# Kernel optimization log

Hardware: AMD Instinct MI355X
Metric: run time of the kernel (lower is better)

Reference implementation:

```python
import jax, jax.numpy as jnp
import numpy as np

N = 10000       # nodes (= number of eigenpairs)
NFEAT = 512
NCLASS = 64     # hidden size of attention/FFN when norm='none'
HID = 128       # feat_encoder hidden
DIM = 32        # eig encoder hidden_dim
K = 10          # outer loop count of ParamNonHarmonicEncoding
NF = DIM // 2   # num_freq = 16
OMEGA = 50.0
DMIN = 0.25
NLAYER = 1


def _ln(x, g, b, eps=1e-5):
    m = jnp.mean(x, axis=-1, keepdims=True)
    v = jnp.mean((x - m) ** 2, axis=-1, keepdims=True)
    return g * (x - m) / jnp.sqrt(v + eps) + b


def setup_inputs() -> dict:
    key = jax.random.key(0)
    ks = jax.random.split(key, 32)
    f32 = jnp.float32
    def w(k, shape, s=0.05):
        return jax.random.normal(k, shape, dtype=f32) * s
    inp = {
        "e": jax.random.uniform(ks[0], (N,), dtype=f32),
        "u": jax.random.normal(ks[1], (N, N), dtype=f32) / np.float32(np.sqrt(N)),
        "x": jax.random.normal(ks[2], (N, NFEAT), dtype=f32),
        # feat_encoder: Linear(nfeat,hid) -> ReLU -> Linear(hid,nclass)
        "fe_w1": w(ks[3], (NFEAT, HID)), "fe_b1": jnp.zeros((HID,), f32),
        "fe_w2": w(ks[4], (HID, NCLASS)), "fe_b2": jnp.zeros((NCLASS,), f32),
        # ParamNonHarmonicEncoding
        "freq_deltas": jax.random.uniform(ks[5], (NF,), dtype=f32) * 0.5,
        "freq_bias": jnp.zeros((), f32),
        "readout_w": w(ks[6], (K, 1 + 2 * NF), 0.1),
        "readout_b": jnp.zeros((K,), f32),
        "alpha_w": w(ks[7], (K, 1), 0.3),   # nn.Linear(k,1,bias=False)
        # mha pre-norm
        "mha_ln_g": jnp.ones((NCLASS,), f32), "mha_ln_b": jnp.zeros((NCLASS,), f32),
        # Diff attention (H=1, hidden=nclass)
        "wq1": w(ks[8], (NCLASS, NCLASS)), "bq1": jnp.zeros((NCLASS,), f32),
        "wk1": w(ks[9], (NCLASS, NCLASS)), "bk1": jnp.zeros((NCLASS,), f32),
        "wq2": w(ks[10], (NCLASS, NCLASS)), "bq2": jnp.zeros((NCLASS,), f32),
        "wk2": w(ks[11], (NCLASS, NCLASS)), "bk2": jnp.zeros((NCLASS,), f32),
        "wv": w(ks[12], (NCLASS, NCLASS)), "bv": jnp.zeros((NCLASS,), f32),
        "lq1": w(ks[13], (NCLASS,), 0.1), "lk1": w(ks[14], (NCLASS,), 0.1),
        "lq2": w(ks[15], (NCLASS,), 0.1), "lk2": w(ks[16], (NCLASS,), 0.1),
        "attn_ln_g": jnp.ones((NCLASS,), f32), "attn_ln_b": jnp.zeros((NCLASS,), f32),
        "out_w": w(ks[17], (NCLASS, NCLASS)), "out_b": jnp.zeros((NCLASS,), f32),
        # gating
        "gate_ln_g": jnp.ones((3 * NCLASS,), f32), "gate_ln_b": jnp.zeros((3 * NCLASS,), f32),
        "gate_w": w(ks[18], (3 * NCLASS, 3)), "gate_b": jnp.zeros((3,), f32),
        # FFN
        "ffn_ln_g": jnp.ones((NCLASS,), f32), "ffn_ln_b": jnp.zeros((NCLASS,), f32),
        "ffn_w1": w(ks[19], (NCLASS, NCLASS)), "ffn_b1": jnp.zeros((NCLASS,), f32),
        "ffn_w2": w(ks[20], (NCLASS, NCLASS)), "ffn_b2": jnp.zeros((NCLASS,), f32),
    }
    return inp


def reference(e, u, x, fe_w1, fe_b1, fe_w2, fe_b2,
              freq_deltas, freq_bias, readout_w, readout_b, alpha_w,
              mha_ln_g, mha_ln_b,
              wq1, bq1, wk1, bk1, wq2, bq2, wk2, bk2, wv, bv,
              lq1, lk1, lq2, lk2, attn_ln_g, attn_ln_b, out_w, out_b,
              gate_ln_g, gate_ln_b, gate_w, gate_b,
              ffn_ln_g, ffn_ln_b, ffn_w1, ffn_b1, ffn_w2, ffn_b2):
    # feat encoder (all dropouts are 0 / eval mode)
    h = jnp.maximum(x @ fe_w1 + fe_b1, 0.0) @ fe_w2 + fe_b2          # [N, C]

    # ParamNonHarmonicEncoding, vectorized over the k powers
    deltas = jax.nn.softplus(freq_deltas) + DMIN
    freqs = jnp.cumsum(deltas) + freq_bias
    freqs = OMEGA * jnp.tanh(freqs / OMEGA)                           # [F]
    powers = e[:, None] ** jnp.arange(1, K + 1, dtype=e.dtype)        # [N, K]
    phase = powers[:, :, None] * freqs                                # [N, K, F]
    ns = jnp.asarray(NF ** 0.5, e.dtype)
    feat = jnp.concatenate(
        [jnp.ones_like(powers)[..., None], jnp.sin(phase) / ns, jnp.cos(phase) / ns],
        axis=-1)                                                      # [N, K, 1+2F]
    eig = jnp.einsum('nkf,kf->nk', feat, readout_w) + readout_b      # [N, K]
    new_e = eig @ alpha_w                                             # [N, 1]

    for layer in range(NLAYER):
        # spectral propagation: u @ diag-like(new_e) @ u^T @ h
        utx = u.T @ h                                                 # [N, C]
        h_fur = u @ (new_e * utx)                                     # [N, C]

        # differential linear attention
        mh = _ln(h, mha_ln_g, mha_ln_b)
        q1 = mh @ wq1 + bq1; k1 = mh @ wk1 + bk1
        q2 = mh @ wq2 + bq2; k2 = mh @ wk2 + bk2
        v = mh @ wv + bv
        k1v = k1.T @ v                                                # [C, C]
        k2v = k2.T @ v
        lam1 = jnp.exp(jnp.sum(lq1 * lk1))
        lam2 = jnp.exp(jnp.sum(lq2 * lk2))
        lam_init = 0.8 - 0.6 * float(np.exp(-0.3 * layer))
        lam_full = lam1 - lam2 + lam_init
        xa = q1 @ k1v - (q2 @ k2v) * lam_full
        xa = _ln(xa, attn_ln_g, attn_ln_b) * (1.0 - lam_init)
        mha_h = xa @ out_w + out_b                                    # [N, C]

        # gated mixing
        cat = jnp.concatenate([h, mha_h, h_fur], axis=-1)             # [N, 3C]
        g = jax.nn.softmax(_ln(cat, gate_ln_g, gate_ln_b) @ gate_w + gate_b, axis=-1)
        mix = h * g[:, 0:1] + mha_h * g[:, 1:2] + h_fur * g[:, 2:3]

        f = _ln(mix, ffn_ln_g, ffn_ln_b)
        f = jax.nn.gelu(f @ ffn_w1 + ffn_b1, approximate=False) @ ffn_w2 + ffn_b2
        h = mix + f
    return h
```

## Files before the change

kernel.cpp:

```cpp
#include <hip/hip_runtime.h>
#include <hip/hip_bf16.h>
#include <math.h>

#define NN 10000
#define J48 10048
#define CHUNKS 157
#define CPS 20
#define SPLITS 8

typedef __bf16 bf16;
typedef bf16 bf16x8 __attribute__((ext_vector_type(8)));
typedef float f32x4 __attribute__((ext_vector_type(4)));

#define SYNC_LDS() do {                                      \
    asm volatile("s_waitcnt lgkmcnt(0)" ::: "memory");       \
    __builtin_amdgcn_sched_barrier(0);                       \
    __builtin_amdgcn_s_barrier();                            \
    __builtin_amdgcn_sched_barrier(0);                       \
  } while (0)

__device__ __forceinline__ float wave_sum64(float v) {
#pragma unroll
  for (int m = 32; m >= 1; m >>= 1) v += __shfl_xor(v, m, 64);
  return v;
}

__global__ void prep_kernel(const float* __restrict__ w1, const float* __restrict__ w2,
                            const float* __restrict__ wq1, const float* __restrict__ wk1,
                            const float* __restrict__ wq2, const float* __restrict__ wk2,
                            const float* __restrict__ wvw,
                            const float* __restrict__ bq1, const float* __restrict__ bk1,
                            const float* __restrict__ bq2, const float* __restrict__ bk2,
                            const float* __restrict__ bvv,
                            const float* __restrict__ lq1, const float* __restrict__ lk1,
                            const float* __restrict__ lq2, const float* __restrict__ lk2,
                            const float* __restrict__ freq_deltas, const float* __restrict__ freq_bias,
                            bf16* __restrict__ w1T, bf16* __restrict__ w2T, bf16* __restrict__ qkvT,
                            float* __restrict__ bqkv, float* __restrict__ freqs, float* __restrict__ lamb) {
  int tid = blockIdx.x * blockDim.x + threadIdx.x;
  int nthr = gridDim.x * blockDim.x;
  for (int i = tid; i < 512 * 128; i += nthr) {
    int o = i >> 9, k = i & 511;
    w1T[i] = (bf16)w1[k * 128 + o];
  }
  for (int i = tid; i < 64 * 128; i += nthr) {
    int o = i >> 7, k = i & 127;
    w2T[i] = (bf16)w2[k * 64 + o];
  }
  for (int i = tid; i < 320 * 64; i += nthr) {
    int r = i >> 6, k = i & 63;
    const float* W = (r < 64) ? wq1 : (r < 128) ? wk1 : (r < 192) ? wq2 : (r < 256) ? wk2 : wvw;
    qkvT[i] = (bf16)W[k * 64 + (r & 63)];
  }
  for (int i = tid; i < 320; i += nthr) {
    const float* B = (i < 64) ? bq1 : (i < 128) ? bk1 : (i < 192) ? bq2 : (i < 256) ? bk2 : bvv;
    bqkv[i] = B[i & 63];
  }
  if (blockIdx.x == 0) {
    if (threadIdx.x == 0) {
      float acc = freq_bias[0];
      for (int f = 0; f < 16; f++) {
        acc += log1pf(expf(freq_deltas[f])) + 0.25f;
        freqs[f] = 50.0f * tanhf(acc * (1.0f / 50.0f));
      }
    }
    if (threadIdx.x >= 64 && threadIdx.x < 128) {
      int l = threadIdx.x - 64;
      float s1 = wave_sum64(lq1[l] * lk1[l]);
      float s2 = wave_sum64(lq2[l] * lk2[l]);
      if (l == 0) lamb[0] = expf(s1) - expf(s2) + 0.2f;
    }
  }
}

__global__ void newe_kernel(const float* __restrict__ e, const float* __restrict__ rw,
                            const float* __restrict__ rb, const float* __restrict__ aw,
                            const float* __restrict__ freqs, float* __restrict__ newe) {
  int n = blockIdx.x * blockDim.x + threadIdx.x;
  if (n >= NN) return;
  float fr[16];
#pragma unroll
  for (int f = 0; f < 16; f++) fr[f] = freqs[f];
  float ev = e[n], p = 1.0f, acc = 0.0f;
  for (int k = 0; k < 10; k++) {
    p *= ev;
    float s = rb[k] + rw[k * 33];
#pragma unroll
    for (int f = 0; f < 16; f++) {
      float ph = p * fr[f];
      s += 0.25f * (__sinf(ph) * rw[k * 33 + 1 + f] + __cosf(ph) * rw[k * 33 + 17 + f]);
    }
    acc += s * aw[k];
  }
  newe[n] = acc;
}

__global__ __launch_bounds__(256) void g1_kernel(const float* __restrict__ x, const bf16* __restrict__ w1T,
                                                 const float* __restrict__ b1, bf16* __restrict__ t1b) {
  __shared__ bf16 la[64][40];
  __shared__ bf16 lb[128][40];
  const int bm = blockIdx.x * 64;
  const int lane = threadIdx.x & 63, wvid = threadIdx.x >> 6;
  const int am = threadIdx.x >> 2, aseg = (threadIdx.x & 3) * 8;
  const int arow = bm + am;
  f32x4 acc[8] = {};
  float4 aLo, aHi;
  uint4 bChunk[2];
  auto fetchAll = [&](int k0) {
    if (arow < NN) {
      const float4* p = (const float4*)(x + (size_t)arow * 512 + k0 + aseg);
      aLo = p[0]; aHi = p[1];
    } else {
      aLo = make_float4(0.f, 0.f, 0.f, 0.f); aHi = aLo;
    }
#pragma unroll
    for (int r = 0; r < 2; r++) {
      int slot = threadIdx.x * 2 + r;
      int n = slot >> 2, seg = (slot & 3) * 8;
      bChunk[r] = *(const uint4*)(w1T + n * 512 + k0 + seg);
    }
  };
  auto store = [&]() {
    union { uint4 v; bf16 b[8]; } pk;
    float av[8] = {aLo.x, aLo.y, aLo.z, aLo.w, aHi.x, aHi.y, aHi.z, aHi.w};
#pragma unroll
    for (int t = 0; t < 8; t++) pk.b[t] = (bf16)av[t];
    *(uint4*)&la[am][aseg] = pk.v;
#pragma unroll
    for (int r = 0; r < 2; r++) {
      int slot = threadIdx.x * 2 + r;
      int n = slot >> 2, seg = (slot & 3) * 8;
      *(uint4*)&lb[n][seg] = bChunk[r];
    }
  };
  fetchAll(0);
  for (int k0 = 0; k0 < 512; k0 += 32) {
    store();
    if (k0 + 32 < 512) fetchAll(k0 + 32);
    __syncthreads();
    bf16x8 af = *(const bf16x8*)&la[wvid * 16 + (lane & 15)][(lane >> 4) * 8];
#pragma unroll
    for (int s = 0; s < 8; s++) {
      bf16x8 bfr = *(const bf16x8*)&lb[s * 16 + (lane & 15)][(lane >> 4) * 8];
      acc[s] = __builtin_amdgcn_mfma_f32_16x16x32_bf16(af, bfr, acc[s], 0, 0, 0);
    }
    __syncthreads();
  }
#pragma unroll
  for (int s = 0; s < 8; s++) {
    int col = s * 16 + (lane & 15);
    float bvv = b1[col];
#pragma unroll
    for (int r = 0; r < 4; r++) {
      int row = bm + wvid * 16 + (lane >> 4) * 4 + r;
      if (row < NN) {
        float v = acc[s][r] + bvv;
        t1b[(size_t)row * 128 + col] = (bf16)(v > 0.f ? v : 0.f);
      }
    }
  }
}

__global__ __launch_bounds__(256) void g2_kernel(const bf16* __restrict__ t1b, const bf16* __restrict__ w2T,
                                                 const float* __restrict__ b2, const float* __restrict__ lng,
                                                 const float* __restrict__ lnb, float* __restrict__ h,
                                                 bf16* __restrict__ hT, bf16* __restrict__ mh) {
  __shared__ bf16 la[64][72];
  __shared__ bf16 lb[64][72];
  const int bm = blockIdx.x * 64;
  const int lane = threadIdx.x & 63, wvid = threadIdx.x >> 6;
  f32x4 acc[4] = {};
  for (int k0 = 0; k0 < 128; k0 += 64) {
#pragma unroll
    for (int r = 0; r < 2; r++) {
      int slot = threadIdx.x * 2 + r;
      int m = slot >> 3, seg = (slot & 7) * 8;
      int row = bm + m;
      uint4 val = make_uint4(0u, 0u, 0u, 0u);
      if (row < NN) val = *(const uint4*)(t1b + (size_t)row * 128 + k0 + seg);
      *(uint4*)&la[m][seg] = val;
      *(uint4*)&lb[m][seg] = *(const uint4*)(w2T + m * 128 + k0 + seg);
    }
    __syncthreads();
#pragma unroll
    for (int ks = 0; ks < 2; ks++) {
      bf16x8 af = *(const bf16x8*)&la[wvid * 16 + (lane & 15)][ks * 32 + (lane >> 4) * 8];
#pragma unroll
      for (int s = 0; s < 4; s++) {
        bf16x8 bfr = *(const bf16x8*)&lb[s * 16 + (lane & 15)][ks * 32 + (lane >> 4) * 8];
        acc[s] = __builtin_amdgcn_mfma_f32_16x16x32_bf16(af, bfr, acc[s], 0, 0, 0);
      }
    }
    __syncthreads();
  }
  float bv4[4], g4[4], lb4[4];
#pragma unroll
  for (int s = 0; s < 4; s++) {
    int col = s * 16 + (lane & 15);
    bv4[s] = b2[col]; g4[s] = lng[col]; lb4[s] = lnb[col];
  }
#pragma unroll
  for (int r = 0; r < 4; r++) {
    float vals[4], psum = 0.f;
#pragma unroll
    for (int s = 0; s < 4; s++) { vals[s] = acc[s][r] + bv4[s]; psum += vals[s]; }
#pragma unroll
    for (int msk = 1; msk < 16; msk <<= 1) psum += __shfl_xor(psum, msk, 64);
    float mean = psum * (1.0f / 64.0f);
    float pvar = 0.f;
#pragma unroll
    for (int s = 0; s < 4; s++) { float dd = vals[s] - mean; pvar += dd * dd; }
#pragma unroll
    for (int msk = 1; msk < 16; msk <<= 1) pvar += __shfl_xor(pvar, msk, 64);
    float rsq = rsqrtf(pvar * (1.0f / 64.0f) + 1e-5f);
    int row = bm + wvid * 16 + (lane >> 4) * 4 + r;
    if (row < NN) {
#pragma unroll
      for (int s = 0; s < 4; s++) {
        int col = s * 16 + (lane & 15);
        float v = vals[s];
        h[(size_t)row * 64 + col] = v;
        hT[(size_t)col * NN + row] = (bf16)v;
        mh[(size_t)row * 64 + col] = (bf16)(g4[s] * (v - mean) * rsq + lb4[s]);
      }
    }
  }
}

__global__ __launch_bounds__(256) void qkv_kernel(const bf16* __restrict__ mh, const bf16* __restrict__ qkvT,
                                                  const float* __restrict__ bqkv,
                                                  bf16* __restrict__ qq, bf16* __restrict__ kv) {
  __shared__ bf16 la[64][72];
  __shared__ bf16 lb[320][72];
  const int bm = blockIdx.x * 64;
  const int lane = threadIdx.x & 63, wvid = threadIdx.x >> 6;
#pragma unroll
  for (int r = 0; r < 2; r++) {
    int slot = threadIdx.x * 2 + r;
    int m = slot >> 3, seg = (slot & 7) * 8;
    int row = bm + m;
    uint4 val = make_uint4(0u, 0u, 0u, 0u);
    if (row < NN) val = *(const uint4*)(mh + (size_t)row * 64 + seg);
    *(uint4*)&la[m][seg] = val;
  }
#pragma unroll
  for (int r = 0; r < 10; r++) {
    int slot = threadIdx.x * 10 + r;
    int n = slot >> 3, seg = (slot & 7) * 8;
    *(uint4*)&lb[n][seg] = *(const uint4*)(qkvT + n * 64 + seg);
  }
  __syncthreads();
  f32x4 acc[20] = {};
#pragma unroll
  for (int ks = 0; ks < 2; ks++) {
    bf16x8 af = *(const bf16x8*)&la[wvid * 16 + (lane & 15)][ks * 32 + (lane >> 4) * 8];
#pragma unroll
    for (int s = 0; s < 20; s++) {
      bf16x8 bfr = *(const bf16x8*)&lb[s * 16 + (lane & 15)][ks * 32 + (lane >> 4) * 8];
      acc[s] = __builtin_amdgcn_mfma_f32_16x16x32_bf16(af, bfr, acc[s], 0, 0, 0);
    }
  }
#pragma unroll
  for (int s = 0; s < 20; s++) {
    int col = s * 16 + (lane & 15);
    float bvv = bqkv[col];
    bf16* dst; int dc, stride;
    if (col < 64)       { dst = qq; dc = col;       stride = 128; }
    else if (col < 128) { dst = kv; dc = col - 64;  stride = 192; }
    else if (col < 192) { dst = qq; dc = col - 64;  stride = 128; }
    else                { dst = kv; dc = col - 128; stride = 192; }
#pragma unroll
    for (int r = 0; r < 4; r++) {
      int row = bm + wvid * 16 + (lane >> 4) * 4 + r;
      if (row < NN) dst[(size_t)row * stride + dc] = (bf16)(acc[s][r] + bvv);
    }
  }
}

__global__ __launch_bounds__(256) void r1_kernel(const bf16* __restrict__ kv, float* __restrict__ part) {
  int b = blockIdx.x;
  int c1 = threadIdx.x & 63, grp = threadIdx.x >> 6;
  int r0 = b * 16;
  float a1[16] = {}, a2[16] = {};
  for (int r = 0; r < 16; r++) {
    const bf16* rowp = kv + (size_t)(r0 + r) * 192;
    float k1 = (float)rowp[c1];
    float k2 = (float)rowp[64 + c1];
    union { uint4 v; bf16 b[8]; } v0, v1;
    v0.v = *(const uint4*)(rowp + 128 + grp * 16);
    v1.v = *(const uint4*)(rowp + 136 + grp * 16);
#pragma unroll
    for (int q = 0; q < 8; q++) {
      float va = (float)v0.b[q], vb = (float)v1.b[q];
      a1[q] += k1 * va; a2[q] += k2 * va;
      a1[8 + q] += k1 * vb; a2[8 + q] += k2 * vb;
    }
  }
  float* p1 = part + (size_t)b * 8192 + (size_t)c1 * 64 + grp * 16;
  float* p2 = p1 + 4096;
#pragma unroll
  for (int q = 0; q < 16; q++) { p1[q] = a1[q]; p2[q] = a2[q]; }
}

__global__ __launch_bounds__(256) void r2a_kernel(const float* __restrict__ part, float* __restrict__ part2) {
  int flat = blockIdx.x * 256 + threadIdx.x;
  int y = blockIdx.y;
  int b0 = y * 79, b1 = min(625, b0 + 79);
  float s = 0.f;
  for (int b = b0; b < b1; b++) s += part[(size_t)b * 8192 + flat];
  part2[(size_t)flat * 8 + y] = s;
}

__global__ void r2b_kernel(const float* __restrict__ part2, const float* __restrict__ lamb, bf16* __restrict__ Bt) {
  int flat = blockIdx.x * 256 + threadIdx.x;
  int mat = flat >> 12, rem = flat & 4095;
  int d = rem >> 6, c = rem & 63;
  f32x4 lo = *(const f32x4*)(part2 + (size_t)flat * 8);
  f32x4 hi = *(const f32x4*)(part2 + (size_t)flat * 8 + 4);
  float s = lo[0] + lo[1] + lo[2] + lo[3] + hi[0] + hi[1] + hi[2] + hi[3];
  float v = mat ? (-lamb[0] * s) : s;
  Bt[c * 128 + mat * 64 + d] = (bf16)v;
}

__global__ __launch_bounds__(256) void d_split_kernel(const float* __restrict__ u, const bf16* __restrict__ hT,
                                                      float* __restrict__ dpart) {
  __shared__ bf16 la[64][72];
  __shared__ bf16 lb[64][72];
  const int j0 = blockIdx.x * 64;
  const int sk = blockIdx.y;
  const int c0 = sk * CPS, c1e = min(CHUNKS, c0 + CPS);
  const int t = threadIdx.x;
  const int lane = t & 63, wv = t >> 6;
  const int jl = (t & 15) * 4;
  const int ir = (t >> 4) * 4;
  f32x4 acc[4] = {};
  uint4 aC[2];
  float4 bC[4];
  auto fetchAll = [&](int i0) {
#pragma unroll
    for (int r = 0; r < 2; r++) {
      int slot = t * 2 + r;
      int c = slot >> 3, seg = (slot & 7) * 8;
      int i = i0 + seg;
      if (i + 7 < NN) aC[r] = *(const uint4*)(hT + (size_t)c * NN + i);
      else {
        union { uint4 v; bf16 b[8]; } tu;
#pragma unroll
        for (int q = 0; q < 8; q++) tu.b[q] = (i + q < NN) ? hT[(size_t)c * NN + i + q] : (bf16)0.f;
        aC[r] = tu.v;
      }
    }
#pragma unroll
    for (int q = 0; q < 4; q++) {
      int i = i0 + ir + q;
      if (i < NN && (j0 + jl + 3) < NN) bC[q] = *(const float4*)(u + (size_t)i * NN + j0 + jl);
      else if (i < NN) {
        float tmp[4];
#pragma unroll
        for (int q2 = 0; q2 < 4; q2++) tmp[q2] = (j0 + jl + q2 < NN) ? u[(size_t)i * NN + j0 + jl + q2] : 0.f;
        bC[q] = make_float4(tmp[0], tmp[1], tmp[2], tmp[3]);
      } else bC[q] = make_float4(0.f, 0.f, 0.f, 0.f);
    }
  };
  auto storeAll = [&]() {
#pragma unroll
    for (int r = 0; r < 2; r++) {
      int slot = t * 2 + r;
      int c = slot >> 3, seg = (slot & 7) * 8;
      *(uint4*)&la[c][seg] = aC[r];
    }
#pragma unroll
    for (int q2 = 0; q2 < 4; q2++) {
      int j = jl + q2;
      int isw = ir ^ (((j >> 2) & 3) << 3);
      union { uint2 w; bf16 b[4]; } pk;
      pk.b[0] = (bf16)((float*)&bC[0])[q2];
      pk.b[1] = (bf16)((float*)&bC[1])[q2];
      pk.b[2] = (bf16)((float*)&bC[2])[q2];
      pk.b[3] = (bf16)((float*)&bC[3])[q2];
      *(uint2*)&lb[j][isw] = pk.w;
    }
  };
  fetchAll(c0 * 64);
  for (int ch = c0; ch < c1e; ch++) {
    storeAll();
    if (ch + 1 < c1e) fetchAll((ch + 1) * 64);
    SYNC_LDS();
#pragma unroll
    for (int ks = 0; ks < 2; ks++) {
      bf16x8 af = *(const bf16x8*)&la[wv * 16 + (lane & 15)][ks * 32 + (lane >> 4) * 8];
#pragma unroll
      for (int s = 0; s < 4; s++) {
        int j = s * 16 + (lane & 15);
        int ioff = (ks * 32 + (lane >> 4) * 8) ^ (((j >> 2) & 3) << 3);
        bf16x8 bfr = *(const bf16x8*)&lb[j][ioff];
        acc[s] = __builtin_amdgcn_mfma_f32_16x16x32_bf16(af, bfr, acc[s], 0, 0, 0);
      }
    }
    SYNC_LDS();
  }
#pragma unroll
  for (int s = 0; s < 4; s++) {
    int j = j0 + s * 16 + (lane & 15);
#pragma unroll
    for (int r = 0; r < 4; r++) {
      int c = wv * 16 + (lane >> 4) * 4 + r;
      dpart[((size_t)sk * 64 + c) * J48 + j] = acc[s][r];
    }
  }
}

__global__ void dred_kernel(const float* __restrict__ dpart, const float* __restrict__ newe,
                            bf16* __restrict__ wutxT) {
  int idx = blockIdx.x * 256 + threadIdx.x;
  int c = idx / 2512;
  int j = (idx - c * 2512) * 4;
  if (c >= 64 || j >= NN) return;
  f32x4 s = {};
  for (int sk = 0; sk < SPLITS; sk++)
    s += *(const f32x4*)(dpart + ((size_t)sk * 64 + c) * J48 + j);
  union { uint2 w; bf16 b[4]; } pk;
#pragma unroll
  for (int q = 0; q < 4; q++) pk.b[q] = (bf16)(newe[j + q] * s[q]);
  *(uint2*)&wutxT[(size_t)c * NN + j] = pk.w;
}

__global__ __launch_bounds__(256) void e_split_kernel(const float* __restrict__ u, const bf16* __restrict__ wutxT,
                                                      float* __restrict__ epart) {
  __shared__ bf16 la[64][72];
  __shared__ bf16 lb[64][72];
  const int bm = blockIdx.x * 64;
  const int sk = blockIdx.y;
  const int c0 = sk * CPS, c1e = min(CHUNKS, c0 + CPS);
  const int t = threadIdx.x;
  const int lane = t & 63, wv = t >> 6;
  const int mA = t >> 2, segA = (t & 3) * 16;
  const int mrow = bm + mA;
  f32x4 acc[4] = {};
  float4 aC[4];
  uint4 bC[2];
  auto fetchAll = [&](int j0) {
    int j = j0 + segA;
    if (mrow < NN && j + 15 < NN) {
      const float4* p = (const float4*)(u + (size_t)mrow * NN + j);
      aC[0] = p[0]; aC[1] = p[1]; aC[2] = p[2]; aC[3] = p[3];
    } else {
#pragma unroll
      for (int q = 0; q < 4; q++) {
        float tmp[4];
#pragma unroll
        for (int q2 = 0; q2 < 4; q2++) {
          int jj = j + q * 4 + q2;
          tmp[q2] = (mrow < NN && jj < NN) ? u[(size_t)mrow * NN + jj] : 0.f;
        }
        aC[q] = make_float4(tmp[0], tmp[1], tmp[2], tmp[3]);
      }
    }
#pragma unroll
    for (int r = 0; r < 2; r++) {
      int slot = t * 2 + r;
      int c = slot >> 3, seg = (slot & 7) * 8;
      int jj = j0 + seg;
      if (jj + 7 < NN) bC[r] = *(const uint4*)(wutxT + (size_t)c * NN + jj);
      else {
        union { uint4 v; bf16 b[8]; } tu;
#pragma unroll
        for (int q = 0; q < 8; q++) tu.b[q] = (jj + q < NN) ? wutxT[(size_t)c * NN + jj + q] : (bf16)0.f;
        bC[r] = tu.v;
      }
    }
  };
  auto storeAll = [&]() {
    union { uint4 v[2]; bf16 b[16]; } pk;
#pragma unroll
    for (int q = 0; q < 4; q++)
#pragma unroll
      for (int q2 = 0; q2 < 4; q2++) pk.b[q * 4 + q2] = (bf16)((float*)&aC[q])[q2];
    *(uint4*)&la[mA][segA] = pk.v[0];
    *(uint4*)&la[mA][segA + 8] = pk.v[1];
#pragma unroll
    for (int r = 0; r < 2; r++) {
      int slot = t * 2 + r;
      int c = slot >> 3, seg = (slot & 7) * 8;
      *(uint4*)&lb[c][seg] = bC[r];
    }
  };
  fetchAll(c0 * 64);
  for (int ch = c0; ch < c1e; ch++) {
    storeAll();
    if (ch + 1 < c1e) fetchAll((ch + 1) * 64);
    SYNC_LDS();
#pragma unroll
    for (int ks = 0; ks < 2; ks++) {
      bf16x8 af = *(const bf16x8*)&la[wv * 16 + (lane & 15)][ks * 32 + (lane >> 4) * 8];
#pragma unroll
      for (int s = 0; s < 4; s++) {
        bf16x8 bfr = *(const bf16x8*)&lb[s * 16 + (lane & 15)][ks * 32 + (lane >> 4) * 8];
        acc[s] = __builtin_amdgcn_mfma_f32_16x16x32_bf16(af, bfr, acc[s], 0, 0, 0);
      }
    }
    SYNC_LDS();
  }
#pragma unroll
  for (int s = 0; s < 4; s++) {
    int col = s * 16 + (lane & 15);
#pragma unroll
    for (int r = 0; r < 4; r++) {
      int row = wv * 16 + (lane >> 4) * 4 + r;
      epart[((size_t)sk * J48 + bm + row) * 64 + col] = acc[s][r];
    }
  }
}

__global__ void ered_kernel(const float* __restrict__ epart, float* __restrict__ h_fur) {
  int idx = blockIdx.x * 256 + threadIdx.x;
  if (idx >= NN * 16) return;
  size_t off = (size_t)idx * 4;
  f32x4 s = {};
  for (int sk = 0; sk < SPLITS; sk++)
    s += *(const f32x4*)(epart + (size_t)sk * (J48 * 64) + off);
  *(f32x4*)(h_fur + off) = s;
}

__global__ __launch_bounds__(256) void hattn_kernel(const bf16* __restrict__ qq, const bf16* __restrict__ Bt,
                                                    const float* __restrict__ g, const float* __restrict__ b,
                                                    bf16* __restrict__ xan) {
  __shared__ bf16 la[64][136];
  __shared__ bf16 lb[64][136];
  const int bm = blockIdx.x * 64;
  const int lane = threadIdx.x & 63, wvid = threadIdx.x >> 6;
#pragma unroll
  for (int r = 0; r < 4; r++) {
    int slot = threadIdx.x * 4 + r;
    int m = slot >> 4, seg = (slot & 15) * 8;
    int row = bm + m;
    uint4 val = make_uint4(0u, 0u, 0u, 0u);
    if (row < NN) val = *(const uint4*)(qq + (size_t)row * 128 + seg);
    *(uint4*)&la[m][seg] = val;
    *(uint4*)&lb[m][seg] = *(const uint4*)(Bt + m * 128 + seg);
  }
  __syncthreads();
  f32x4 acc[4] = {};
#pragma unroll
  for (int ks = 0; ks < 4; ks++) {
    bf16x8 af = *(const bf16x8*)&la[wvid * 16 + (lane & 15)][ks * 32 + (lane >> 4) * 8];
#pragma unroll
    for (int s = 0; s < 4; s++) {
      bf16x8 bfr = *(const bf16x8*)&lb[s * 16 + (lane & 15)][ks * 32 + (lane >> 4) * 8];
      acc[s] = __builtin_amdgcn_mfma_f32_16x16x32_bf16(af, bfr, acc[s], 0, 0, 0);
    }
  }
#pragma unroll
  for (int r = 0; r < 4; r++) {
    float psum = acc[0][r] + acc[1][r] + acc[2][r] + acc[3][r];
#pragma unroll
    for (int msk = 1; msk < 16; msk <<= 1) psum += __shfl_xor(psum, msk, 64);
    float mean = psum * (1.0f / 64.0f);
    float pvar = 0.f;
#pragma unroll
    for (int s = 0; s < 4; s++) { float dd = acc[s][r] - mean; pvar += dd * dd; }
#pragma unroll
    for (int msk = 1; msk < 16; msk <<= 1) pvar += __shfl_xor(pvar, msk, 64);
    float rsq = rsqrtf(pvar * (1.0f / 64.0f) + 1e-5f);
    int row = bm + wvid * 16 + (lane >> 4) * 4 + r;
    if (row < NN) {
#pragma unroll
      for (int s = 0; s < 4; s++) {
        int col = s * 16 + (lane & 15);
        float o = 0.8f * (g[col] * (acc[s][r] - mean) * rsq + b[col]);
        xan[(size_t)row * 64 + col] = (bf16)o;
      }
    }
  }
}

__global__ __launch_bounds__(256) void final_kernel(const float* __restrict__ h, const float* __restrict__ h_fur,
                                                    const bf16* __restrict__ xan,
                                                    const float* __restrict__ out_w, const float* __restrict__ out_b,
                                                    const float* __restrict__ gg, const float* __restrict__ gb,
                                                    const float* __restrict__ gw, const float* __restrict__ gbias,
                                                    const float* __restrict__ fg, const float* __restrict__ fb,
                                                    const float* __restrict__ fw1, const float* __restrict__ fb1,
                                                    const float* __restrict__ fw2, const float* __restrict__ fb2,
                                                    float* __restrict__ out) {
  __shared__ float s_ow[64][64];
  __shared__ float s_w1[64][64];
  __shared__ float s_w2[64][64];
  __shared__ float s_gw[192][3];
  __shared__ float s_row[4][64];
  const int lane = threadIdx.x & 63, wvid = threadIdx.x >> 6;
  for (int i = threadIdx.x; i < 4096; i += 256) {
    ((float*)s_ow)[i] = out_w[i];
    ((float*)s_w1)[i] = fw1[i];
    ((float*)s_w2)[i] = fw2[i];
  }
  for (int i = threadIdx.x; i < 576; i += 256) ((float*)s_gw)[i] = gw[i];
  const int row = blockIdx.x * 4 + wvid;
  float x_h = h[(size_t)row * 64 + lane];
  float x_f = h_fur[(size_t)row * 64 + lane];
  float x_a = (float)xan[(size_t)row * 64 + lane];
  s_row[wvid][lane] = x_a;
  __syncthreads();
  float mha = out_b[lane];
#pragma unroll 8
  for (int d = 0; d < 64; d++) mha += s_row[wvid][d] * s_ow[d][lane];
  float m3 = wave_sum64(x_h + mha + x_f) * (1.0f / 192.0f);
  float dh = x_h - m3, dm = mha - m3, df = x_f - m3;
  float v3 = wave_sum64(dh * dh + dm * dm + df * df) * (1.0f / 192.0f);
  float rs3 = rsqrtf(v3 + 1e-5f);
  float l0 = gg[lane] * dh * rs3 + gb[lane];
  float l1 = gg[64 + lane] * dm * rs3 + gb[64 + lane];
  float l2 = gg[128 + lane] * df * rs3 + gb[128 + lane];
  float p0 = l0 * s_gw[lane][0] + l1 * s_gw[64 + lane][0] + l2 * s_gw[128 + lane][0];
  float p1 = l0 * s_gw[lane][1] + l1 * s_gw[64 + lane][1] + l2 * s_gw[128 + lane][1];
  float p2 = l0 * s_gw[lane][2] + l1 * s_gw[64 + lane][2] + l2 * s_gw[128 + lane][2];
  p0 = wave_sum64(p0) + gbias[0];
  p1 = wave_sum64(p1) + gbias[1];
  p2 = wave_sum64(p2) + gbias[2];
  float mx = fmaxf(p0, fmaxf(p1, p2));
  float e0 = expf(p0 - mx), e1 = expf(p1 - mx), e2 = expf(p2 - mx);
  float inv = 1.0f / (e0 + e1 + e2);
  float mix = x_h * (e0 * inv) + mha * (e1 * inv) + x_f * (e2 * inv);
  float mf = wave_sum64(mix) * (1.0f / 64.0f);
  float dmx = mix - mf;
  float vf = wave_sum64(dmx * dmx) * (1.0f / 64.0f);
  float f = fg[lane] * dmx * rsqrtf(vf + 1e-5f) + fb[lane];
  __syncthreads();
  s_row[wvid][lane] = f;
  __syncthreads();
  float t1 = fb1[lane];
#pragma unroll 8
  for (int d = 0; d < 64; d++) t1 += s_row[wvid][d] * s_w1[d][lane];
  t1 = 0.5f * t1 * (1.0f + erff(t1 * 0.70710678118654752f));
  __syncthreads();
  s_row[wvid][lane] = t1;
  __syncthreads();
  float f2 = fb2[lane];
#pragma unroll 8
  for (int d = 0; d < 64; d++) f2 += s_row[wvid][d] * s_w2[d][lane];
  out[(size_t)row * 64 + lane] = mix + f2;
}

extern "C" void kernel_launch(void* const* d_in, const int* in_sizes, int n_in,
                              void* d_out, int out_size, void* d_ws, size_t ws_size,
                              hipStream_t stream) {
  const float* e          = (const float*)d_in[0];
  const float* u          = (const float*)d_in[1];
  const float* x          = (const float*)d_in[2];
  const float* fe_w1      = (const float*)d_in[3];
  const float* fe_b1      = (const float*)d_in[4];
  const float* fe_w2      = (const float*)d_in[5];
  const float* fe_b2      = (const float*)d_in[6];
  const float* freq_deltas= (const float*)d_in[7];
  const float* freq_bias  = (const float*)d_in[8];
  const float* readout_w  = (const float*)d_in[9];
  const float* readout_b  = (const float*)d_in[10];
  const float* alpha_w    = (const float*)d_in[11];
  const float* mha_ln_g   = (const float*)d_in[12];
  const float* mha_ln_b   = (const float*)d_in[13];
  const float* wq1        = (const float*)d_in[14];
  const float* bq1        = (const float*)d_in[15];
  const float* wk1        = (const float*)d_in[16];
  const float* bk1        = (const float*)d_in[17];
  const float* wq2        = (const float*)d_in[18];
  const float* bq2        = (const float*)d_in[19];
  const float* wk2        = (const float*)d_in[20];
  const float* bk2        = (const float*)d_in[21];
  const float* wv_in      = (const float*)d_in[22];
  const float* bv_in      = (const float*)d_in[23];
  const float* lq1        = (const float*)d_in[24];
  const float* lk1        = (const float*)d_in[25];
  const float* lq2        = (const float*)d_in[26];
  const float* lk2        = (const float*)d_in[27];
  const float* attn_ln_g  = (const float*)d_in[28];
  const float* attn_ln_b  = (const float*)d_in[29];
  const float* out_w      = (const float*)d_in[30];
  const float* out_b      = (const float*)d_in[31];
  const float* gate_ln_g  = (const float*)d_in[32];
  const float* gate_ln_b  = (const float*)d_in[33];
  const float* gate_w     = (const float*)d_in[34];
  const float* gate_b     = (const float*)d_in[35];
  const float* ffn_ln_g   = (const float*)d_in[36];
  const float* ffn_ln_b   = (const float*)d_in[37];
  const float* ffn_w1     = (const float*)d_in[38];
  const float* ffn_b1     = (const float*)d_in[39];
  const float* ffn_w2     = (const float*)d_in[40];
  const float* ffn_b2     = (const float*)d_in[41];

  constexpr size_t OFF_H     = 0;
  constexpr size_t OFF_T1B   = 2560000;
  constexpr size_t OFF_HT    = 5120000;
  constexpr size_t OFF_MH    = 6400000;
  constexpr size_t OFF_QQ    = 7680000;
  constexpr size_t OFF_KV    = 10240000;
  constexpr size_t OFF_WUTXT = 14080000;
  constexpr size_t OFF_HFUR  = 15360000;
  constexpr size_t OFF_XAN   = 17920000;
  constexpr size_t OFF_NEWE  = 19200000;
  constexpr size_t OFF_BT    = 19240064;
  constexpr size_t OFF_W1T   = 19256448;
  constexpr size_t OFF_W2T   = 19387520;
  constexpr size_t OFF_QKVT  = 19403904;
  constexpr size_t OFF_BQKV  = 19444864;
  constexpr size_t OFF_FREQS = 19446144;
  constexpr size_t OFF_LAM   = 19446208;
  constexpr size_t OFF_BIG   = 19446272;
  constexpr size_t SZ_SPART  = (size_t)SPLITS * 64 * J48 * 4;
  constexpr size_t OFF_PART2 = OFF_BIG + SZ_SPART;
  constexpr size_t WS_NEED   = OFF_PART2 + 262144;
  if (ws_size < WS_NEED) return;

  char* ws = (char*)d_ws;
  float* h_buf   = (float*)(ws + OFF_H);
  bf16*  t1b     = (bf16*)(ws + OFF_T1B);
  bf16*  hT      = (bf16*)(ws + OFF_HT);
  bf16*  mh      = (bf16*)(ws + OFF_MH);
  bf16*  qq      = (bf16*)(ws + OFF_QQ);
  bf16*  kv      = (bf16*)(ws + OFF_KV);
  bf16*  wutxT   = (bf16*)(ws + OFF_WUTXT);
  float* h_fur   = (float*)(ws + OFF_HFUR);
  bf16*  xan     = (bf16*)(ws + OFF_XAN);
  float* newe    = (float*)(ws + OFF_NEWE);
  bf16*  Bt      = (bf16*)(ws + OFF_BT);
  bf16*  w1T     = (bf16*)(ws + OFF_W1T);
  bf16*  w2T     = (bf16*)(ws + OFF_W2T);
  bf16*  qkvT    = (bf16*)(ws + OFF_QKVT);
  float* bqkv    = (float*)(ws + OFF_BQKV);
  float* freqs   = (float*)(ws + OFF_FREQS);
  float* lamb    = (float*)(ws + OFF_LAM);
  float* part    = (float*)(ws + OFF_BIG);
  float* part2   = (float*)(ws + OFF_PART2);
  float* dpart   = (float*)(ws + OFF_BIG);
  float* epart   = (float*)(ws + OFF_BIG);

  prep_kernel<<<64, 256, 0, stream>>>(fe_w1, fe_w2, wq1, wk1, wq2, wk2, wv_in,
                                      bq1, bk1, bq2, bk2, bv_in,
                                      lq1, lk1, lq2, lk2, freq_deltas, freq_bias,
                                      w1T, w2T, qkvT, bqkv, freqs, lamb);
  newe_kernel<<<40, 256, 0, stream>>>(e, readout_w, readout_b, alpha_w, freqs, newe);
  g1_kernel<<<157, 256, 0, stream>>>(x, w1T, fe_b1, t1b);
  g2_kernel<<<157, 256, 0, stream>>>(t1b, w2T, fe_b2, mha_ln_g, mha_ln_b, h_buf, hT, mh);
  qkv_kernel<<<157, 256, 0, stream>>>(mh, qkvT, bqkv, qq, kv);
  r1_kernel<<<625, 256, 0, stream>>>(kv, part);
  r2a_kernel<<<dim3(32, 8), 256, 0, stream>>>(part, part2);
  r2b_kernel<<<32, 256, 0, stream>>>(part2, lamb, Bt);
  d_split_kernel<<<dim3(157, SPLITS), 256, 0, stream>>>(u, hT, dpart);
  dred_kernel<<<628, 256, 0, stream>>>(dpart, newe, wutxT);
  e_split_kernel<<<dim3(157, SPLITS), 256, 0, stream>>>(u, wutxT, epart);
  ered_kernel<<<625, 256, 0, stream>>>(epart, h_fur);
  hattn_kernel<<<157, 256, 0, stream>>>(qq, Bt, attn_ln_g, attn_ln_b, xan);
  final_kernel<<<2500, 256, 0, stream>>>(h_buf, h_fur, xan, out_w, out_b,
                                         gate_ln_g, gate_ln_b, gate_w, gate_b,
                                         ffn_ln_g, ffn_ln_b, ffn_w1, ffn_b1, ffn_w2, ffn_b2,
                                         (float*)d_out);
}
```

Before: 361.1 us.

## Restructure U@W GEMM with wide coalesced row loads and fuse split-K reduce into final

```diff
diff --git a/kernel.cpp b/kernel.cpp
--- a/kernel.cpp
+++ b/kernel.cpp
@@ -11,13 +11,6 @@
 typedef __bf16 bf16;
 typedef bf16 bf16x8 __attribute__((ext_vector_type(8)));
 typedef float f32x4 __attribute__((ext_vector_type(4)));
-
-#define SYNC_LDS() do {                                      \
-    asm volatile("s_waitcnt lgkmcnt(0)" ::: "memory");       \
-    __builtin_amdgcn_sched_barrier(0);                       \
-    __builtin_amdgcn_s_barrier();                            \
-    __builtin_amdgcn_sched_barrier(0);                       \
-  } while (0)
 
 __device__ __forceinline__ float wave_sum64(float v) {
 #pragma unroll
@@ -385,7 +378,7 @@
   for (int ch = c0; ch < c1e; ch++) {
     storeAll();
     if (ch + 1 < c1e) fetchAll((ch + 1) * 64);
-    SYNC_LDS();
+    __syncthreads();
 #pragma unroll
     for (int ks = 0; ks < 2; ks++) {
       bf16x8 af = *(const bf16x8*)&la[wv * 16 + (lane & 15)][ks * 32 + (lane >> 4) * 8];
@@ -397,7 +390,7 @@
         acc[s] = __builtin_amdgcn_mfma_f32_16x16x32_bf16(af, bfr, acc[s], 0, 0, 0);
       }
     }
-    SYNC_LDS();
+    __syncthreads();
   }
 #pragma unroll
   for (int s = 0; s < 4; s++) {
@@ -425,81 +418,66 @@
   *(uint2*)&wutxT[(size_t)c * NN + j] = pk.w;
 }
 
-__global__ __launch_bounds__(256) void e_split_kernel(const float* __restrict__ u, const bf16* __restrict__ wutxT,
-                                                      float* __restrict__ epart) {
-  __shared__ bf16 la[64][72];
+__global__ __launch_bounds__(256) void e4_kernel(const float* __restrict__ u, const bf16* __restrict__ wutxT,
+                                                 float* __restrict__ epart) {
+  __shared__ bf16 la[64][264];
   __shared__ bf16 lb[64][72];
   const int bm = blockIdx.x * 64;
   const int sk = blockIdx.y;
-  const int c0 = sk * CPS, c1e = min(CHUNKS, c0 + CPS);
   const int t = threadIdx.x;
   const int lane = t & 63, wv = t >> 6;
-  const int mA = t >> 2, segA = (t & 3) * 16;
-  const int mrow = bm + mA;
+  const int jl = (t & 63) * 4;
   f32x4 acc[4] = {};
-  float4 aC[4];
-  uint4 bC[2];
-  auto fetchAll = [&](int j0) {
-    int j = j0 + segA;
-    if (mrow < NN && j + 15 < NN) {
-      const float4* p = (const float4*)(u + (size_t)mrow * NN + j);
-      aC[0] = p[0]; aC[1] = p[1]; aC[2] = p[2]; aC[3] = p[3];
-    } else {
-#pragma unroll
-      for (int q = 0; q < 4; q++) {
+  for (int cj = sk * 5; cj < sk * 5 + 5; cj++) {
+    const int jg0 = cj * 256;
+#pragma unroll
+    for (int is = 0; is < 16; is++) {
+      int il = is * 4 + wv;
+      int i = bm + il;
+      int j = jg0 + jl;
+      float4 v;
+      if (i < NN && j + 3 < NN) v = *(const float4*)(u + (size_t)i * NN + j);
+      else if (i < NN) {
         float tmp[4];
 #pragma unroll
-        for (int q2 = 0; q2 < 4; q2++) {
-          int jj = j + q * 4 + q2;
-          tmp[q2] = (mrow < NN && jj < NN) ? u[(size_t)mrow * NN + jj] : 0.f;
+        for (int q2 = 0; q2 < 4; q2++) tmp[q2] = (j + q2 < NN) ? u[(size_t)i * NN + j + q2] : 0.f;
+        v = make_float4(tmp[0], tmp[1], tmp[2], tmp[3]);
+      } else v = make_float4(0.f, 0.f, 0.f, 0.f);
+      union { uint w[2]; bf16 b[4]; } pk;
+      pk.b[0] = (bf16)v.x; pk.b[1] = (bf16)v.y; pk.b[2] = (bf16)v.z; pk.b[3] = (bf16)v.w;
+      *(uint2*)&la[il][jl ^ ((il & 7) << 3)] = *(const uint2*)pk.w;
+    }
+#pragma unroll
+    for (int inner = 0; inner < 4; inner++) {
+#pragma unroll
+      for (int r = 0; r < 2; r++) {
+        int slot = t * 2 + r;
+        int c = slot >> 3, seg = (slot & 7) * 8;
+        int jj = jg0 + inner * 64 + seg;
+        uint4 v;
+        if (jj + 7 < NN) v = *(const uint4*)(wutxT + (size_t)c * NN + jj);
+        else {
+          union { uint4 v; bf16 b[8]; } tu;
+#pragma unroll
+          for (int q = 0; q < 8; q++) tu.b[q] = (jj + q < NN) ? wutxT[(size_t)c * NN + jj + q] : (bf16)0.f;
+          v = tu.v;
         }
-        aC[q] = make_float4(tmp[0], tmp[1], tmp[2], tmp[3]);
-      }
-    }
-#pragma unroll
-    for (int r = 0; r < 2; r++) {
-      int slot = t * 2 + r;
-      int c = slot >> 3, seg = (slot & 7) * 8;
-      int jj = j0 + seg;
-      if (jj + 7 < NN) bC[r] = *(const uint4*)(wutxT + (size_t)c * NN + jj);
-      else {
-        union { uint4 v; bf16 b[8]; } tu;
-#pragma unroll
-        for (int q = 0; q < 8; q++) tu.b[q] = (jj + q < NN) ? wutxT[(size_t)c * NN + jj + q] : (bf16)0.f;
-        bC[r] = tu.v;
-      }
-    }
-  };
-  auto storeAll = [&]() {
-    union { uint4 v[2]; bf16 b[16]; } pk;
-#pragma unroll
-    for (int q = 0; q < 4; q++)
-#pragma unroll
-      for (int q2 = 0; q2 < 4; q2++) pk.b[q * 4 + q2] = (bf16)((float*)&aC[q])[q2];
-    *(uint4*)&la[mA][segA] = pk.v[0];
-    *(uint4*)&la[mA][segA + 8] = pk.v[1];
-#pragma unroll
-    for (int r = 0; r < 2; r++) {
-      int slot = t * 2 + r;
-      int c = slot >> 3, seg = (slot & 7) * 8;
-      *(uint4*)&lb[c][seg] = bC[r];
-    }
-  };
-  fetchAll(c0 * 64);
-  for (int ch = c0; ch < c1e; ch++) {
-    storeAll();
-    if (ch + 1 < c1e) fetchAll((ch + 1) * 64);
-    SYNC_LDS();
-#pragma unroll
-    for (int ks = 0; ks < 2; ks++) {
-      bf16x8 af = *(const bf16x8*)&la[wv * 16 + (lane & 15)][ks * 32 + (lane >> 4) * 8];
-#pragma unroll
-      for (int s = 0; s < 4; s++) {
-        bf16x8 bfr = *(const bf16x8*)&lb[s * 16 + (lane & 15)][ks * 32 + (lane >> 4) * 8];
-        acc[s] = __builtin_amdgcn_mfma_f32_16x16x32_bf16(af, bfr, acc[s], 0, 0, 0);
-      }
-    }
-    SYNC_LDS();
+        *(uint4*)&lb[c][seg] = v;
+      }
+      __syncthreads();
+#pragma unroll
+      for (int ks = 0; ks < 2; ks++) {
+        int il = wv * 16 + (lane & 15);
+        int joff = (inner * 64 + ks * 32 + (lane >> 4) * 8) ^ ((il & 7) << 3);
+        bf16x8 af = *(const bf16x8*)&la[il][joff];
+#pragma unroll
+        for (int s = 0; s < 4; s++) {
+          bf16x8 bfr = *(const bf16x8*)&lb[s * 16 + (lane & 15)][ks * 32 + (lane >> 4) * 8];
+          acc[s] = __builtin_amdgcn_mfma_f32_16x16x32_bf16(af, bfr, acc[s], 0, 0, 0);
+        }
+      }
+      __syncthreads();
+    }
   }
 #pragma unroll
   for (int s = 0; s < 4; s++) {
@@ -510,16 +488,6 @@
       epart[((size_t)sk * J48 + bm + row) * 64 + col] = acc[s][r];
     }
   }
-}
-
-__global__ void ered_kernel(const float* __restrict__ epart, float* __restrict__ h_fur) {
-  int idx = blockIdx.x * 256 + threadIdx.x;
-  if (idx >= NN * 16) return;
-  size_t off = (size_t)idx * 4;
-  f32x4 s = {};
-  for (int sk = 0; sk < SPLITS; sk++)
-    s += *(const f32x4*)(epart + (size_t)sk * (J48 * 64) + off);
-  *(f32x4*)(h_fur + off) = s;
 }
 
 __global__ __launch_bounds__(256) void hattn_kernel(const bf16* __restrict__ qq, const bf16* __restrict__ Bt,
@@ -574,7 +542,7 @@
   }
 }
 
-__global__ __launch_bounds__(256) void final_kernel(const float* __restrict__ h, const float* __restrict__ h_fur,
+__global__ __launch_bounds__(256) void final_kernel(const float* __restrict__ h, const float* __restrict__ epart,
                                                     const bf16* __restrict__ xan,
                                                     const float* __restrict__ out_w, const float* __restrict__ out_b,
                                                     const float* __restrict__ gg, const float* __restrict__ gb,
@@ -597,7 +565,10 @@
   for (int i = threadIdx.x; i < 576; i += 256) ((float*)s_gw)[i] = gw[i];
   const int row = blockIdx.x * 4 + wvid;
   float x_h = h[(size_t)row * 64 + lane];
-  float x_f = h_fur[(size_t)row * 64 + lane];
+  float x_f = 0.f;
+#pragma unroll
+  for (int sk = 0; sk < SPLITS; sk++)
+    x_f += epart[((size_t)sk * J48 + row) * 64 + lane];
   float x_a = (float)xan[(size_t)row * 64 + lane];
   s_row[wvid][lane] = x_a;
   __syncthreads();
@@ -694,7 +665,6 @@
   constexpr size_t OFF_QQ    = 7680000;
   constexpr size_t OFF_KV    = 10240000;
   constexpr size_t OFF_WUTXT = 14080000;
-  constexpr size_t OFF_HFUR  = 15360000;
   constexpr size_t OFF_XAN   = 17920000;
   constexpr size_t OFF_NEWE  = 19200000;
   constexpr size_t OFF_BT    = 19240064;
@@ -718,7 +688,6 @@
   bf16*  qq      = (bf16*)(ws + OFF_QQ);
   bf16*  kv      = (bf16*)(ws + OFF_KV);
   bf16*  wutxT   = (bf16*)(ws + OFF_WUTXT);
-  float* h_fur   = (float*)(ws + OFF_HFUR);
   bf16*  xan     = (bf16*)(ws + OFF_XAN);
   float* newe    = (float*)(ws + OFF_NEWE);
   bf16*  Bt      = (bf16*)(ws + OFF_BT);
@@ -746,10 +715,9 @@
   r2b_kernel<<<32, 256, 0, stream>>>(part2, lamb, Bt);
   d_split_kernel<<<dim3(157, SPLITS), 256, 0, stream>>>(u, hT, dpart);
   dred_kernel<<<628, 256, 0, stream>>>(dpart, newe, wutxT);
-  e_split_kernel<<<dim3(157, SPLITS), 256, 0, stream>>>(u, wutxT, epart);
-  ered_kernel<<<625, 256, 0, stream>>>(epart, h_fur);
+  e4_kernel<<<dim3(157, SPLITS), 256, 0, stream>>>(u, wutxT, epart);
   hattn_kernel<<<157, 256, 0, stream>>>(qq, Bt, attn_ln_g, attn_ln_b, xan);
-  final_kernel<<<2500, 256, 0, stream>>>(h_buf, h_fur, xan, out_w, out_b,
+  final_kernel<<<2500, 256, 0, stream>>>(h_buf, epart, xan, out_w, out_b,
                                          gate_ln_g, gate_ln_b, gate_w, gate_b,
                                          ffn_ln_g, ffn_ln_b, ffn_w1, ffn_b1, ffn_w2, ffn_b2,
                                          (float*)d_out);
```

Result: slower. 390.6 us (+8.2%).
